# Kernel optimization log

Measured on AMD Instinct MI355X. Metric: run time of the kernel, lower is better.

The kernel has to match this reference:

```python
import jax, jax.numpy as jnp
import numpy as np

NUM_LATENTS = 1
NUM_EMBEDDINGS = 2048
EMBEDDING_DIM = 64
DECAY = 0.99
EPS = 1e-5


def setup_inputs() -> dict:
    key = jax.random.key(0)
    k1, k2 = jax.random.split(key)
    x = jax.random.normal(k1, (65536, NUM_LATENTS * EMBEDDING_DIM), dtype=jnp.float32)
    embedding = jax.random.normal(k2, (NUM_LATENTS, NUM_EMBEDDINGS, EMBEDDING_DIM), dtype=jnp.float32)
    cluster_size = jnp.ones((NUM_LATENTS, NUM_EMBEDDINGS), dtype=jnp.float32)
    return {"input": x, "embedding": embedding, "cluster_size": cluster_size}


def reference(input, embedding, cluster_size):
    L, K, D = embedding.shape
    flat = input.reshape(-1, L, D)  # (N, L, D)
    # Squared euclidean distances (N, L, K), expanded form of (x - e)^2 sum over D
    x_sq = jnp.sum(flat * flat, axis=-1, keepdims=True)           # (N, L, 1)
    e_sq = jnp.sum(embedding * embedding, axis=-1)[None]          # (1, L, K)
    cross = jnp.einsum('nld,lkd->nlk', flat, embedding)           # (N, L, K)
    distances = x_sq - 2.0 * cross + e_sq
    encoding_indices = jnp.argmin(distances, axis=-1)             # (N, L)
    # decode: gather codebook vectors
    quantized = embedding[jnp.arange(L)[None, :], encoding_indices]  # (N, L, D)
    encodings = jax.nn.one_hot(encoding_indices, K, dtype=input.dtype)  # (N, L, K)
    # --- EMA update (training branch, non-simple, laplace smoothing) ---
    onehot_sum = jnp.sum(encodings, axis=0)                       # (L, K)
    dw = jnp.einsum('nlk,nld->lkd', encodings, flat)              # (L, K, D)
    new_cluster_size = DECAY * cluster_size + (1.0 - DECAY) * onehot_sum
    n = jnp.sum(new_cluster_size, axis=-1, keepdims=True)
    cs = (new_cluster_size + EPS) / (n + K * EPS) * n
    new_embedding = DECAY * embedding + (1.0 - DECAY) * (dw / cs[..., None])
    # --- losses / outputs ---
    q = quantized.reshape(input.shape)
    commitment_loss = jnp.mean((q - input) ** 2)
    quantized_st = input + jax.lax.stop_gradient(q - input)
    avg_probs = jnp.mean(encodings, axis=0)                       # (L, K)
    perplexity = jnp.exp(-jnp.sum(avg_probs * jnp.log(avg_probs + 1e-10) / L))
    return (quantized_st, encodings, commitment_loss, perplexity, new_embedding, new_cluster_size)
```

## Files before the change

kernel.cpp:

```cpp
#include <hip/hip_runtime.h>
#include <math.h>

#define NROWS 65536
#define KEMB  2048
#define DIM   64
#define DECAYF 0.99f
#define OMDF   0.01f
#define EPSF   1e-5f

#define WS_DW    0
#define WS_CNT   131072
#define WS_LOSS  133120
#define WS_ESQ   133632
#define WS_SCALE 135680
#define WS_IDX   137728
#define WS_SORT  203264
#define WS_START 268800
#define WS_CUR   270852

#define OUT_Q    0
#define OUT_ENC  4194304
#define OUT_LOSS 138412032
#define OUT_PERP 138412033
#define OUT_NE   138412034
#define OUT_NCS  138543106

typedef float f32x4 __attribute__((ext_vector_type(4)));

__global__ __launch_bounds__(256) void k0_prep(const float* __restrict__ E,
                                               float* __restrict__ ws) {
    int g = blockIdx.x * 256 + threadIdx.x;
    if (g == 0) ws[WS_LOSS] = 0.f;
    ((float4*)(ws + WS_DW))[g] = make_float4(0.f, 0.f, 0.f, 0.f);
    if (g < KEMB) {
        ((unsigned int*)ws)[WS_CNT + g] = 0u;
        const float4* e4 = (const float4*)(E + (size_t)g * DIM);
        float s0 = 0.f, s1 = 0.f, s2 = 0.f, s3 = 0.f;
#pragma unroll
        for (int j = 0; j < 16; j++) {
            float4 v = e4[j];
            s0 = fmaf(v.x, v.x, s0); s1 = fmaf(v.y, v.y, s1);
            s2 = fmaf(v.z, v.z, s2); s3 = fmaf(v.w, v.w, s3);
        }
        ws[WS_ESQ + g] = (s0 + s1) + (s2 + s3);
    }
}

__global__ __launch_bounds__(256, 2) void k1_main(const float* __restrict__ x,
                                                  const float* __restrict__ E,
                                                  float* __restrict__ ws,
                                                  float* __restrict__ out) {
    __shared__ float sxT[64 * 128];
    __shared__ float seT[32 * 256];
    __shared__ float sxq[256];

    const int t = threadIdx.x;
    const int b = blockIdx.x;
    const int tx = t & 15;
    const int ty = t >> 4;

    {
        const int rl = t & 127;
        const int dhi2 = t >> 7;
        const float4* x4 = (const float4*)x;
        float s0 = 0.f, s1 = 0.f, s2 = 0.f, s3 = 0.f;
#pragma unroll
        for (int i = 0; i < 8; i++) {
            int dc = dhi2 + 2 * i;
            float4 v = x4[((size_t)b * 128 + rl) * 16 + dc];
            sxT[(4 * dc + 0) * 128 + rl] = v.x;
            sxT[(4 * dc + 1) * 128 + rl] = v.y;
            sxT[(4 * dc + 2) * 128 + rl] = v.z;
            sxT[(4 * dc + 3) * 128 + rl] = v.w;
            s0 = fmaf(v.x, v.x, s0); s1 = fmaf(v.y, v.y, s1);
            s2 = fmaf(v.z, v.z, s2); s3 = fmaf(v.w, v.w, s3);
        }
        sxq[dhi2 * 128 + rl] = (s0 + s1) + (s2 + s3);
    }

    const int sbase = (((t >> 2) & 3) << 6) + ((t >> 4) << 2) + (t & 3);
    const float4* e4 = (const float4*)E;

    float4 pv[8];
#pragma unroll
    for (int j = 0; j < 8; j++)
        pv[j] = e4[(size_t)t * 16 + j];

    __syncthreads();

    float xsq[8];
#pragma unroll
    for (int rr = 0; rr < 8; rr++)
        xsq[rr] = sxq[ty * 8 + rr] + sxq[128 + ty * 8 + rr];

    float best[8];
    int bidx[8];
#pragma unroll
    for (int rr = 0; rr < 8; rr++) { best[rr] = 3.4e38f; bidx[rr] = 0; }

    f32x4* __restrict__ encz = (f32x4*)(out + OUT_ENC);

    for (int pass = 0; pass < 8; pass++) {
        float acc[8][16];
#pragma unroll
        for (int rr = 0; rr < 8; rr++)
#pragma unroll
            for (int m = 0; m < 16; m++) acc[rr][m] = 0.f;

        for (int dh = 0; dh < 2; dh++) {
            if (pass + dh) __syncthreads();
#pragma unroll
            for (int j = 0; j < 8; j++) {
                seT[(4 * j + 0) * 256 + sbase] = pv[j].x;
                seT[(4 * j + 1) * 256 + sbase] = pv[j].y;
                seT[(4 * j + 2) * 256 + sbase] = pv[j].z;
                seT[(4 * j + 3) * 256 + sbase] = pv[j].w;
            }
            __syncthreads();

            {
                int h = pass * 2 + dh + 1;
                if (h < 16) {
#pragma unroll
                    for (int j = 0; j < 8; j++)
                        pv[j] = e4[((size_t)((h >> 1) * 256 + t)) * 16 + (h & 1) * 8 + j];
                }
            }

            if (dh == 0) {
                f32x4 z = (f32x4)(0.f);
#pragma unroll
                for (int j = 0; j < 32; j++)
                    __builtin_nontemporal_store(z,
                        encz + (size_t)b * 65536 + pass * 8192 + j * 256 + t);
            }

            const float* xbase = sxT + dh * 32 * 128 + ty * 8;
            for (int dd = 0; dd < 32; dd++) {
                const float* sb = seT + dd * 256;
                f32x4 a0 = *(const f32x4*)(xbase + dd * 128);
                f32x4 a1 = *(const f32x4*)(xbase + dd * 128 + 4);
                f32x4 b0 = *(const f32x4*)(sb + tx * 4);
                f32x4 b1 = *(const f32x4*)(sb + 64 + tx * 4);
                f32x4 b2 = *(const f32x4*)(sb + 128 + tx * 4);
                f32x4 b3 = *(const f32x4*)(sb + 192 + tx * 4);
#pragma unroll
                for (int rr = 0; rr < 4; rr++) {
#pragma unroll
                    for (int cc = 0; cc < 4; cc++) {
                        acc[rr][cc]          = fmaf(a0[rr], b0[cc], acc[rr][cc]);
                        acc[rr][4 + cc]      = fmaf(a0[rr], b1[cc], acc[rr][4 + cc]);
                        acc[rr][8 + cc]      = fmaf(a0[rr], b2[cc], acc[rr][8 + cc]);
                        acc[rr][12 + cc]     = fmaf(a0[rr], b3[cc], acc[rr][12 + cc]);
                        acc[4 + rr][cc]      = fmaf(a1[rr], b0[cc], acc[4 + rr][cc]);
                        acc[4 + rr][4 + cc]  = fmaf(a1[rr], b1[cc], acc[4 + rr][4 + cc]);
                        acc[4 + rr][8 + cc]  = fmaf(a1[rr], b2[cc], acc[4 + rr][8 + cc]);
                        acc[4 + rr][12 + cc] = fmaf(a1[rr], b3[cc], acc[4 + rr][12 + cc]);
                    }
                }
            }
        }

        const float4* esq4 = (const float4*)(ws + WS_ESQ + pass * 256 + tx * 16);
        float4 eqv0 = esq4[0], eqv1 = esq4[1], eqv2 = esq4[2], eqv3 = esq4[3];
        float eq[16] = {eqv0.x, eqv0.y, eqv0.z, eqv0.w, eqv1.x, eqv1.y, eqv1.z, eqv1.w,
                        eqv2.x, eqv2.y, eqv2.z, eqv2.w, eqv3.x, eqv3.y, eqv3.z, eqv3.w};
        const int kb = pass * 256 + tx * 16;
#pragma unroll
        for (int rr = 0; rr < 8; rr++)
#pragma unroll
            for (int m = 0; m < 16; m++) {
                float dist = fmaf(-2.f, acc[rr][m], xsq[rr]) + eq[m];
                if (dist < best[rr]) { best[rr] = dist; bidx[rr] = kb + m; }
            }
    }

    __syncthreads();
    int* sIdx = (int*)sxq;
#pragma unroll
    for (int rr = 0; rr < 8; rr++) {
        float bd = best[rr]; int bi = bidx[rr];
#pragma unroll
        for (int m = 1; m < 16; m <<= 1) {
            float od = __shfl_xor(bd, m, 64);
            int   oi = __shfl_xor(bi, m, 64);
            if (od < bd || (od == bd && oi < bi)) { bd = od; bi = oi; }
        }
        if (tx == 0) sIdx[ty * 8 + rr] = bi;
    }
    __syncthreads();

    if (t < 128) {
        const int row = b * 128 + t;
        const int bi = sIdx[t];
        ((int*)ws)[WS_IDX + row] = bi;
        atomicAdd(((unsigned int*)ws) + WS_CNT + bi, 1u);
        out[OUT_ENC + (size_t)row * KEMB + bi] = 1.0f;
        const float4* ebb = (const float4*)(E + (size_t)bi * DIM);
        const float4* xr4 = (const float4*)(x + (size_t)row * DIM);
        float4* qo = (float4*)(out + OUT_Q + (size_t)row * DIM);
        float l0 = 0.f, l1 = 0.f, l2 = 0.f, l3 = 0.f;
#pragma unroll
        for (int j = 0; j < 16; j++) {
            float4 ev = ebb[j];
            float4 xv = xr4[j];
            qo[j] = ev;
            float d0 = ev.x - xv.x, d1 = ev.y - xv.y;
            float d2 = ev.z - xv.z, d3 = ev.w - xv.w;
            l0 = fmaf(d0, d0, l0); l1 = fmaf(d1, d1, l1);
            l2 = fmaf(d2, d2, l2); l3 = fmaf(d3, d3, l3);
        }
        float lsum = (l0 + l1) + (l2 + l3);
#pragma unroll
        for (int o = 32; o; o >>= 1) lsum += __shfl_down(lsum, o, 64);
        if ((t & 63) == 0) unsafeAtomicAdd(ws + WS_LOSS, lsum);
    }
}

__global__ __launch_bounds__(256) void k2bs(const float* __restrict__ cs_in,
                                            float* __restrict__ ws,
                                            float* __restrict__ out) {
    __shared__ unsigned int sscan[256];
    __shared__ float sred[8];
    __shared__ float s_n;
    const int t = threadIdx.x;
    const unsigned int* cnt = ((const unsigned int*)ws) + WS_CNT;

    unsigned int c[8];
    unsigned int tot = 0;
#pragma unroll
    for (int j = 0; j < 8; j++) { c[j] = cnt[t * 8 + j]; tot += c[j]; }
    sscan[t] = tot;
    __syncthreads();
    for (int off = 1; off < 256; off <<= 1) {
        unsigned int v = (t >= off) ? sscan[t - off] : 0u;
        __syncthreads();
        sscan[t] += v;
        __syncthreads();
    }
    unsigned int run = sscan[t] - tot;
    unsigned int* starts = ((unsigned int*)ws) + WS_START;
    unsigned int* cur = ((unsigned int*)ws) + WS_CUR;
#pragma unroll
    for (int j = 0; j < 8; j++) {
        starts[t * 8 + j] = run;
        cur[t * 8 + j] = run;
        run += c[j];
    }
    if (t == 255) starts[KEMB] = run;

    float* ncs_out = out + OUT_NCS;
    float ln = 0.f, lent = 0.f;
    float ncs_v[8];
#pragma unroll
    for (int j = 0; j < 8; j++) {
        int k = t * 8 + j;
        float cf = (float)c[j];
        float ncs = DECAYF * cs_in[k] + OMDF * cf;
        ncs_out[k] = ncs;
        ncs_v[j] = ncs;
        ln += ncs;
        float p = cf * (1.0f / 65536.0f);
        lent = fmaf(p, logf(p + 1e-10f), lent);
    }
#pragma unroll
    for (int o = 32; o; o >>= 1) {
        ln += __shfl_down(ln, o, 64);
        lent += __shfl_down(lent, o, 64);
    }
    if ((t & 63) == 0) { sred[t >> 6] = ln; sred[4 + (t >> 6)] = lent; }
    __syncthreads();
    if (t == 0) {
        float n = (sred[0] + sred[1]) + (sred[2] + sred[3]);
        float ent = (sred[4] + sred[5]) + (sred[6] + sred[7]);
        s_n = n;
        out[OUT_LOSS] = ws[WS_LOSS] * (1.0f / 4194304.0f);
        out[OUT_PERP] = expf(-ent);
    }
    __syncthreads();
    float n = s_n;
    float denom = n + (float)KEMB * EPSF;
#pragma unroll
    for (int j = 0; j < 8; j++) {
        int k = t * 8 + j;
        float cs = (ncs_v[j] + EPSF) / denom * n;
        ws[WS_SCALE + k] = OMDF / cs;
    }
}

__global__ __launch_bounds__(256) void k2c_scatter(const int* __restrict__ idxp,
                                                   float* __restrict__ ws) {
    const int g = blockIdx.x * 256 + threadIdx.x;
    int4 v = ((const int4*)idxp)[g];
    unsigned int* cur = ((unsigned int*)ws) + WS_CUR;
    int* sorted = ((int*)ws) + WS_SORT;
    const int row = 4 * g;
    unsigned int p0 = atomicAdd(&cur[v.x], 1u);
    unsigned int p1 = atomicAdd(&cur[v.y], 1u);
    unsigned int p2 = atomicAdd(&cur[v.z], 1u);
    unsigned int p3 = atomicAdd(&cur[v.w], 1u);
    sorted[p0] = row + 0;
    sorted[p1] = row + 1;
    sorted[p2] = row + 2;
    sorted[p3] = row + 3;
}

__global__ __launch_bounds__(256) void k2d_dw(const float* __restrict__ x,
                                              const int* __restrict__ idxp,
                                              float* __restrict__ ws) {
    const int t = threadIdx.x;
    const int lane = t & 63;
    const int w = blockIdx.x * 4 + (t >> 6);
    const int base = w * 64;
    const int* sorted = ((const int*)ws) + WS_SORT;

    int rid = sorted[base + lane];
    int code_l = idxp[rid];

    float acc = 0.f;
    int cur = __shfl(code_l, 0, 64);
#pragma unroll 8
    for (int i = 0; i < 64; i++) {
        int row = __shfl(rid, i, 64);
        int code = __shfl(code_l, i, 64);
        if (code != cur) {
            unsafeAtomicAdd(ws + WS_DW + (size_t)cur * DIM + lane, acc);
            acc = 0.f;
            cur = code;
        }
        acc += x[(size_t)row * DIM + lane];
    }
    unsafeAtomicAdd(ws + WS_DW + (size_t)cur * DIM + lane, acc);
}

__global__ __launch_bounds__(256) void k4_embed(const float* __restrict__ E,
                                                const float* __restrict__ ws,
                                                float* __restrict__ out) {
    int gq = blockIdx.x * 256 + threadIdx.x;
    const float4* E4 = (const float4*)E;
    const float4* dw4 = (const float4*)(ws + WS_DW);
    float2* o2 = (float2*)(out + OUT_NE);
    int k = gq >> 4;
    float sc = ws[WS_SCALE + k];
    float4 e = E4[gq];
    float4 d = dw4[gq];
    float2 r0, r1;
    r0.x = fmaf(d.x, sc, DECAYF * e.x);
    r0.y = fmaf(d.y, sc, DECAYF * e.y);
    r1.x = fmaf(d.z, sc, DECAYF * e.z);
    r1.y = fmaf(d.w, sc, DECAYF * e.w);
    o2[2 * gq + 0] = r0;
    o2[2 * gq + 1] = r1;
}

extern "C" void kernel_launch(void* const* d_in, const int* in_sizes, int n_in,
                              void* d_out, int out_size, void* d_ws, size_t ws_size,
                              hipStream_t stream) {
    const float* x = (const float*)d_in[0];
    const float* E = (const float*)d_in[1];
    const float* cs = (const float*)d_in[2];
    float* out = (float*)d_out;
    float* ws = (float*)d_ws;
    const int* idxp = ((const int*)ws) + WS_IDX;

    hipLaunchKernelGGL(k0_prep, dim3(128), dim3(256), 0, stream, E, ws);
    hipLaunchKernelGGL(k1_main, dim3(512), dim3(256), 0, stream, x, E, ws, out);
    hipLaunchKernelGGL(k2bs, dim3(1), dim3(256), 0, stream, cs, ws, out);
    hipLaunchKernelGGL(k2c_scatter, dim3(64), dim3(256), 0, stream, idxp, ws);
    hipLaunchKernelGGL(k2d_dw, dim3(256), dim3(256), 0, stream, x, idxp, ws);
    hipLaunchKernelGGL(k4_embed, dim3(128), dim3(256), 0, stream, E, ws, out);
}
```

Baseline: 295.9 us.

## Accumulate dw with atomics in main kernel and fuse EMA finalize kernels

The main kernel's epilogue now adds each input row straight into its code's dw slot with float atomics. This removes the index buffer, the counting-sort scatter and the segmented-reduction kernel. The scan/stats kernel and the embedding-update kernel are merged into one 128-block kernel, and every block recomputes the global cluster-size sum itself. Launch count drops from six to three, at the cost of 64 uncoalesced float atomics per row inside the main kernel. A __syncthreads before the shared index staging was also removed, which could introduce a race if that shared buffer is still being read.

```diff
diff --git a/kernel.cpp b/kernel.cpp
--- a/kernel.cpp
+++ b/kernel.cpp
@@ -12,11 +12,6 @@
 #define WS_CNT   131072
 #define WS_LOSS  133120
 #define WS_ESQ   133632
-#define WS_SCALE 135680
-#define WS_IDX   137728
-#define WS_SORT  203264
-#define WS_START 268800
-#define WS_CUR   270852
 
 #define OUT_Q    0
 #define OUT_ENC  4194304
@@ -175,7 +170,6 @@
             }
     }
 
-    __syncthreads();
     int* sIdx = (int*)sxq;
 #pragma unroll
     for (int rr = 0; rr < 8; rr++) {
@@ -193,18 +187,22 @@
     if (t < 128) {
         const int row = b * 128 + t;
         const int bi = sIdx[t];
-        ((int*)ws)[WS_IDX + row] = bi;
         atomicAdd(((unsigned int*)ws) + WS_CNT + bi, 1u);
         out[OUT_ENC + (size_t)row * KEMB + bi] = 1.0f;
         const float4* ebb = (const float4*)(E + (size_t)bi * DIM);
         const float4* xr4 = (const float4*)(x + (size_t)row * DIM);
         float4* qo = (float4*)(out + OUT_Q + (size_t)row * DIM);
+        float* dwp = ws + WS_DW + (size_t)bi * DIM;
         float l0 = 0.f, l1 = 0.f, l2 = 0.f, l3 = 0.f;
 #pragma unroll
         for (int j = 0; j < 16; j++) {
             float4 ev = ebb[j];
             float4 xv = xr4[j];
             qo[j] = ev;
+            unsafeAtomicAdd(dwp + 4 * j + 0, xv.x);
+            unsafeAtomicAdd(dwp + 4 * j + 1, xv.y);
+            unsafeAtomicAdd(dwp + 4 * j + 2, xv.z);
+            unsafeAtomicAdd(dwp + 4 * j + 3, xv.w);
             float d0 = ev.x - xv.x, d1 = ev.y - xv.y;
             float d2 = ev.z - xv.z, d3 = ev.w - xv.w;
             l0 = fmaf(d0, d0, l0); l1 = fmaf(d1, d1, l1);
@@ -217,50 +215,25 @@
     }
 }
 
-__global__ __launch_bounds__(256) void k2bs(const float* __restrict__ cs_in,
-                                            float* __restrict__ ws,
-                                            float* __restrict__ out) {
-    __shared__ unsigned int sscan[256];
+__global__ __launch_bounds__(256) void k2_se(const float* __restrict__ cs_in,
+                                             const float* __restrict__ E,
+                                             const float* __restrict__ ws,
+                                             float* __restrict__ out) {
     __shared__ float sred[8];
+    __shared__ float sscale[16];
     __shared__ float s_n;
     const int t = threadIdx.x;
+    const int b = blockIdx.x;
     const unsigned int* cnt = ((const unsigned int*)ws) + WS_CNT;
 
-    unsigned int c[8];
-    unsigned int tot = 0;
-#pragma unroll
-    for (int j = 0; j < 8; j++) { c[j] = cnt[t * 8 + j]; tot += c[j]; }
-    sscan[t] = tot;
-    __syncthreads();
-    for (int off = 1; off < 256; off <<= 1) {
-        unsigned int v = (t >= off) ? sscan[t - off] : 0u;
-        __syncthreads();
-        sscan[t] += v;
-        __syncthreads();
-    }
-    unsigned int run = sscan[t] - tot;
-    unsigned int* starts = ((unsigned int*)ws) + WS_START;
-    unsigned int* cur = ((unsigned int*)ws) + WS_CUR;
-#pragma unroll
-    for (int j = 0; j < 8; j++) {
-        starts[t * 8 + j] = run;
-        cur[t * 8 + j] = run;
-        run += c[j];
-    }
-    if (t == 255) starts[KEMB] = run;
-
-    float* ncs_out = out + OUT_NCS;
     float ln = 0.f, lent = 0.f;
-    float ncs_v[8];
 #pragma unroll
     for (int j = 0; j < 8; j++) {
         int k = t * 8 + j;
-        float cf = (float)c[j];
-        float ncs = DECAYF * cs_in[k] + OMDF * cf;
-        ncs_out[k] = ncs;
-        ncs_v[j] = ncs;
+        float c = (float)cnt[k];
+        float ncs = DECAYF * cs_in[k] + OMDF * c;
         ln += ncs;
-        float p = cf * (1.0f / 65536.0f);
+        float p = c * (1.0f / 65536.0f);
         lent = fmaf(p, logf(p + 1e-10f), lent);
     }
 #pragma unroll
@@ -274,83 +247,38 @@
         float n = (sred[0] + sred[1]) + (sred[2] + sred[3]);
         float ent = (sred[4] + sred[5]) + (sred[6] + sred[7]);
         s_n = n;
-        out[OUT_LOSS] = ws[WS_LOSS] * (1.0f / 4194304.0f);
-        out[OUT_PERP] = expf(-ent);
-    }
-    __syncthreads();
-    float n = s_n;
-    float denom = n + (float)KEMB * EPSF;
-#pragma unroll
-    for (int j = 0; j < 8; j++) {
-        int k = t * 8 + j;
-        float cs = (ncs_v[j] + EPSF) / denom * n;
-        ws[WS_SCALE + k] = OMDF / cs;
-    }
-}
-
-__global__ __launch_bounds__(256) void k2c_scatter(const int* __restrict__ idxp,
-                                                   float* __restrict__ ws) {
-    const int g = blockIdx.x * 256 + threadIdx.x;
-    int4 v = ((const int4*)idxp)[g];
-    unsigned int* cur = ((unsigned int*)ws) + WS_CUR;
-    int* sorted = ((int*)ws) + WS_SORT;
-    const int row = 4 * g;
-    unsigned int p0 = atomicAdd(&cur[v.x], 1u);
-    unsigned int p1 = atomicAdd(&cur[v.y], 1u);
-    unsigned int p2 = atomicAdd(&cur[v.z], 1u);
-    unsigned int p3 = atomicAdd(&cur[v.w], 1u);
-    sorted[p0] = row + 0;
-    sorted[p1] = row + 1;
-    sorted[p2] = row + 2;
-    sorted[p3] = row + 3;
-}
-
-__global__ __launch_bounds__(256) void k2d_dw(const float* __restrict__ x,
-                                              const int* __restrict__ idxp,
-                                              float* __restrict__ ws) {
-    const int t = threadIdx.x;
-    const int lane = t & 63;
-    const int w = blockIdx.x * 4 + (t >> 6);
-    const int base = w * 64;
-    const int* sorted = ((const int*)ws) + WS_SORT;
-
-    int rid = sorted[base + lane];
-    int code_l = idxp[rid];
-
-    float acc = 0.f;
-    int cur = __shfl(code_l, 0, 64);
-#pragma unroll 8
-    for (int i = 0; i < 64; i++) {
-        int row = __shfl(rid, i, 64);
-        int code = __shfl(code_l, i, 64);
-        if (code != cur) {
-            unsafeAtomicAdd(ws + WS_DW + (size_t)cur * DIM + lane, acc);
-            acc = 0.f;
-            cur = code;
-        }
-        acc += x[(size_t)row * DIM + lane];
-    }
-    unsafeAtomicAdd(ws + WS_DW + (size_t)cur * DIM + lane, acc);
-}
-
-__global__ __launch_bounds__(256) void k4_embed(const float* __restrict__ E,
-                                                const float* __restrict__ ws,
-                                                float* __restrict__ out) {
-    int gq = blockIdx.x * 256 + threadIdx.x;
-    const float4* E4 = (const float4*)E;
-    const float4* dw4 = (const float4*)(ws + WS_DW);
+        if (b == 0) {
+            out[OUT_LOSS] = ws[WS_LOSS] * (1.0f / 4194304.0f);
+            out[OUT_PERP] = expf(-ent);
+        }
+    }
+    __syncthreads();
+    const float n = s_n;
+
+    if (t < 16) {
+        int k = b * 16 + t;
+        float c = (float)cnt[k];
+        float ncs = DECAYF * cs_in[k] + OMDF * c;
+        out[OUT_NCS + k] = ncs;
+        float cs = (ncs + EPSF) / (n + (float)KEMB * EPSF) * n;
+        sscale[t] = OMDF / cs;
+    }
+    __syncthreads();
+
+    const int k16 = t >> 4;
+    const int d = (t & 15) * 4;
+    const int k = b * 16 + k16;
+    const float sc = sscale[k16];
+    float4 e = ((const float4*)E)[k * 16 + (t & 15)];
+    float4 dv = ((const float4*)(ws + WS_DW))[k * 16 + (t & 15)];
+    float2 r0, r1;
+    r0.x = fmaf(dv.x, sc, DECAYF * e.x);
+    r0.y = fmaf(dv.y, sc, DECAYF * e.y);
+    r1.x = fmaf(dv.z, sc, DECAYF * e.z);
+    r1.y = fmaf(dv.w, sc, DECAYF * e.w);
     float2* o2 = (float2*)(out + OUT_NE);
-    int k = gq >> 4;
-    float sc = ws[WS_SCALE + k];
-    float4 e = E4[gq];
-    float4 d = dw4[gq];
-    float2 r0, r1;
-    r0.x = fmaf(d.x, sc, DECAYF * e.x);
-    r0.y = fmaf(d.y, sc, DECAYF * e.y);
-    r1.x = fmaf(d.z, sc, DECAYF * e.z);
-    r1.y = fmaf(d.w, sc, DECAYF * e.w);
-    o2[2 * gq + 0] = r0;
-    o2[2 * gq + 1] = r1;
+    o2[(k * 64 + d) / 2 + 0] = r0;
+    o2[(k * 64 + d) / 2 + 1] = r1;
 }
 
 extern "C" void kernel_launch(void* const* d_in, const int* in_sizes, int n_in,
@@ -361,12 +289,8 @@
     const float* cs = (const float*)d_in[2];
     float* out = (float*)d_out;
     float* ws = (float*)d_ws;
-    const int* idxp = ((const int*)ws) + WS_IDX;
 
     hipLaunchKernelGGL(k0_prep, dim3(128), dim3(256), 0, stream, E, ws);
     hipLaunchKernelGGL(k1_main, dim3(512), dim3(256), 0, stream, x, E, ws, out);
-    hipLaunchKernelGGL(k2bs, dim3(1), dim3(256), 0, stream, cs, ws, out);
-    hipLaunchKernelGGL(k2c_scatter, dim3(64), dim3(256), 0, stream, idxp, ws);
-    hipLaunchKernelGGL(k2d_dw, dim3(256), dim3(256), 0, stream, x, idxp, ws);
-    hipLaunchKernelGGL(k4_embed, dim3(128), dim3(256), 0, stream, E, ws, out);
-}
+    hipLaunchKernelGGL(k2_se, dim3(128), dim3(256), 0, stream, cs, E, ws, out);
+}
```

Measured after the change: 869.6 us. 2.94x slower.
